# Kernel tuning notes

Hardware: AMD Instinct MI355X
Metric: run time of the kernel (lower is better)

The kernel has to match this reference:

```python
import jax, jax.numpy as jnp
import numpy as np
import math

H = 16
SEG = 128
DIL = 2


def hilbert_perm(M: int) -> jnp.ndarray:
    # Boustrophedon (snake) traversal of a ceil(sqrt(M)) grid, matching
    # create_hilbert_mapping_simple: skip linear positions >= M, keep first M.
    g = int(math.ceil(math.sqrt(M)))
    grid = np.arange(g * g).reshape(g, g)
    grid[1::2] = grid[1::2, ::-1]
    flat = grid.reshape(-1)
    flat = flat[flat < M][:M]
    return jnp.asarray(flat, dtype=jnp.int32)


def setup_inputs() -> dict:
    key = jax.random.key(0)
    kx, kq, ko = jax.random.split(key, 3)
    B, M, D = 4, 4096, 1024
    x = jax.random.normal(kx, (B, M, D), dtype=jnp.float32)
    # nn.Linear weights: [out_features, in_features], y = x @ W.T
    w_qkv = jax.random.normal(kq, (3 * D, D), dtype=jnp.float32) * (D ** -0.5)
    w_out = jax.random.normal(ko, (D, D), dtype=jnp.float32) * (D ** -0.5)
    return {"x": x, "w_qkv": w_qkv, "w_out": w_out}


def reference(x, w_qkv, w_out):
    B, M, Dm = x.shape
    hd = Dm // H
    scale = hd ** -0.5
    S = M // SEG  # number of segments (M chosen as a multiple of SEG)

    qkv = x @ w_qkv.T                              # [B, M, 3*Dm]
    qkv = qkv.reshape(B, M, 3, H, hd)
    q = qkv[:, :, 0].transpose(0, 2, 1, 3)         # [B, H, M, hd]
    k = qkv[:, :, 1].transpose(0, 2, 1, 3)
    v = qkv[:, :, 2].transpose(0, 2, 1, 3)

    perm = hilbert_perm(M)
    qh = q[:, :, perm]                             # Hilbert-reordered
    kh = k[:, :, perm]
    vh = v[:, :, perm]

    # segment-local dilated attention: each query attends to keys at
    # positions seg_start + j*DIL within its own segment
    qh = qh.reshape(B, H, S, SEG, hd)
    kd = kh.reshape(B, H, S, SEG, hd)[:, :, :, ::DIL]   # [B,H,S,SEG//DIL,hd]
    vd = vh.reshape(B, H, S, SEG, hd)[:, :, :, ::DIL]

    scores = jnp.einsum('bhsqd,bhskd->bhsqk', qh * scale, kd)
    attn = jax.nn.softmax(scores, axis=-1)
    o = jnp.einsum('bhsqk,bhskd->bhsqd', attn, vd)       # [B,H,S,SEG,hd]
    o = o.reshape(B, H, M, hd).transpose(0, 2, 1, 3).reshape(B, M, Dm)
    return o @ w_out.T
```

## Files before the change

kernel.cpp:

```cpp
#include <hip/hip_runtime.h>


typedef _Float16 f16x8 __attribute__((ext_vector_type(8)));
typedef _Float16 f16x4 __attribute__((ext_vector_type(4)));
typedef float f32x4 __attribute__((ext_vector_type(4)));

__device__ __forceinline__ int hperm(int i) {
  int r = i >> 6, c = i & 63;
  return (r << 6) | ((r & 1) ? (63 - c) : c);
}
__device__ __forceinline__ int arow_gather(int mp) {
  int b = mp >> 11, i = mp & 2047;
  int s = i >> 6, j = i & 63;
  return b * 4096 + hperm(s * 128 + 2 * j);
}
__device__ __forceinline__ void gload_lds16(const _Float16* g, _Float16* l) {
  __builtin_amdgcn_global_load_lds(
      (const __attribute__((address_space(1))) void*)g,
      (__attribute__((address_space(3))) void*)l, 16, 0, 0);
}

__global__ __launch_bounds__(256) void cast_all(
    const float* __restrict__ x, _Float16* __restrict__ xh,
    const float* __restrict__ wq, _Float16* __restrict__ wqh,
    const float* __restrict__ wo, _Float16* __restrict__ woh) {
  for (int i = blockIdx.x * 256 + threadIdx.x; i < 5242880; i += 256 * 2048) {
    const float* s;
    _Float16* d;
    int j;
    if (i < 4194304) {
      s = x; d = xh; j = i;
    } else if (i < 4980736) {
      s = wq; d = wqh; j = i - 4194304;
    } else {
      s = wo; d = woh; j = i - 4980736;
    }
    float4 v = ((const float4*)s)[j];
    f16x4 o;
    o[0] = (_Float16)v.x;
    o[1] = (_Float16)v.y;
    o[2] = (_Float16)v.z;
    o[3] = (_Float16)v.w;
    *(f16x4*)&d[(size_t)j * 4] = o;
  }
}


#define BAR __builtin_amdgcn_s_barrier()
#define LGKM_(n)                                            \
  do {                                                      \
    asm volatile("s_waitcnt lgkmcnt(" #n ")" ::: "memory"); \
    __builtin_amdgcn_sched_barrier(0);                      \
  } while (0)
#define VM4 asm volatile("s_waitcnt vmcnt(4)" ::: "memory")
#define VM0 asm volatile("s_waitcnt vmcnt(0)" ::: "memory")

#define STG(mat, kt, h, buf)                                               \
  do {                                                                     \
    const _Float16* g0 = ((mat) ? gpB : gpA)[(h)*2] + (size_t)(kt)*64;     \
    const _Float16* g1 = ((mat) ? gpB : gpA)[(h)*2 + 1] + (size_t)(kt)*64; \
    _Float16* d_ = &lds[buf][mat][h][t * 8];                               \
    gload_lds16(g0, d_);                                                   \
    gload_lds16(g1, d_ + 4096);                                            \
  } while (0)

#define LDA_K(buf, mh, ks)                                     \
  _Pragma("unroll") for (int m = 0; m < 4; m++) a[ks][m] =     \
      *(const f16x8*)(aB[buf][ks] + (mh)*4096 + m * 1024);

#define LDB_K(buf, nh, ks)                                           \
  _Pragma("unroll") for (int nf = 0; nf < 2; nf++) b[nh][ks][nf] =   \
      *(const f16x8*)(bB[buf][ks] + (nh)*2048 + nf * 1024);

#define MMH(mh, nh, ks)                                                     \
  _Pragma("unroll") for (int m = 0; m < 4; m++)                             \
      _Pragma("unroll") for (int nf = 0; nf < 2; nf++)                      \
          acc[(mh)*4 + m][(nh)*2 + nf] =                                    \
              __builtin_amdgcn_mfma_f32_16x16x32_f16(                       \
                  a[ks][m], b[nh][ks][nf], acc[(mh)*4 + m][(nh)*2 + nf],    \
                  0, 0, 0);

#define STQ(mh, nh)                                                        \
  _Pragma("unroll") for (int mf = 0; mf < 4; mf++) {                       \
    size_t row0 = arow0 + wm * 128 + ((mh)*4 + mf) * 16 + lg * 4;          \
    _Pragma("unroll") for (int nf = 0; nf < 2; nf++) {                     \
      size_t col = brow0 + wn * 64 + ((nh)*2 + nf) * 16 + lr;              \
      _Pragma("unroll") for (int j = 0; j < 4; j++) {                      \
        OutT v_ = (OutT)acc[(mh)*4 + mf][(nh)*2 + nf][j];                  \
        if constexpr (NT)                                                  \
          __builtin_nontemporal_store(v_, &C[(row0 + j) * N + col]);       \
        else                                                               \
          C[(row0 + j) * N + col] = v_;                                    \
      }                                                                    \
    }                                                                      \
  }

template <typename OutT, bool NT>
__device__ __forceinline__ void gemm_body(
    const _Float16* const* gpA, const _Float16* const* gpB,
    OutT* __restrict__ C, int N, size_t arow0, size_t brow0,
    _Float16 (&lds)[2][2][2][8192]) {
  const int t = threadIdx.x;
  const int lane = t & 63, wave = t >> 6;
  const int wm = wave >> 2, wn = wave & 3;
  const int lr = lane & 15, lg = lane >> 4;

  const int cx0 = (lg * 8) ^ ((lr & 7) << 3);
  const int cx1 = cx0 ^ 32;
  const _Float16* aB[2][2];
  const _Float16* bB[2][2];
#pragma unroll
  for (int bf = 0; bf < 2; bf++) {
    aB[bf][0] = &lds[bf][0][wm][lr * 64 + cx0];
    aB[bf][1] = &lds[bf][0][wm][lr * 64 + cx1];
    bB[bf][0] = &lds[bf][1][wn >> 1][(wn & 1) * 4096 + lr * 64 + cx0];
    bB[bf][1] = &lds[bf][1][wn >> 1][(wn & 1) * 4096 + lr * 64 + cx1];
  }

  f32x4 acc[8][4] = {};
  f16x8 a[2][4], b[2][2][2];

  STG(0, 0, 0, 0);
  STG(0, 0, 1, 0);
  STG(1, 0, 0, 0);
  STG(1, 0, 1, 0);
  STG(1, 1, 0, 1);
  STG(1, 1, 1, 1);
  VM4;
  BAR;

  for (int i = 0; i < 7; i++) {
    const int k1 = 2 * i + 1, k2 = 2 * i + 2, k3 = 2 * i + 3;
    LDA_K(0, 0, 0); LDB_K(0, 0, 0); LDA_K(0, 0, 1); LDB_K(0, 0, 1);
    STG(0, k1, 0, 1); BAR; LGKM_(6); MMH(0, 0, 0); LGKM_(0); MMH(0, 0, 1);
    LDB_K(0, 1, 0); LDB_K(0, 1, 1);
    STG(0, k1, 1, 1); BAR; LGKM_(2); MMH(0, 1, 0); LGKM_(0); MMH(0, 1, 1);
    LDA_K(0, 1, 0); LDA_K(0, 1, 1);
    STG(1, k2, 0, 0); BAR; LGKM_(4); MMH(1, 1, 0); LGKM_(0); MMH(1, 1, 1);
    STG(1, k2, 1, 0); VM4; BAR; MMH(1, 0, 0); MMH(1, 0, 1);
    LDA_K(1, 0, 0); LDB_K(1, 0, 0); LDA_K(1, 0, 1); LDB_K(1, 0, 1);
    STG(0, k2, 0, 0); BAR; LGKM_(6); MMH(0, 0, 0); LGKM_(0); MMH(0, 0, 1);
    LDB_K(1, 1, 0); LDB_K(1, 1, 1);
    STG(0, k2, 1, 0); BAR; LGKM_(2); MMH(0, 1, 0); LGKM_(0); MMH(0, 1, 1);
    LDA_K(1, 1, 0); LDA_K(1, 1, 1);
    STG(1, k3, 0, 1); BAR; LGKM_(4); MMH(1, 1, 0); LGKM_(0); MMH(1, 1, 1);
    STG(1, k3, 1, 1); VM4; BAR; MMH(1, 0, 0); MMH(1, 0, 1);
  }

  {
    LDA_K(0, 0, 0); LDB_K(0, 0, 0); LDA_K(0, 0, 1); LDB_K(0, 0, 1);
    STG(0, 15, 0, 1); BAR; LGKM_(6); MMH(0, 0, 0); LGKM_(0); MMH(0, 0, 1);
    LDB_K(0, 1, 0); LDB_K(0, 1, 1);
    STG(0, 15, 1, 1); BAR; LGKM_(2); MMH(0, 1, 0); LGKM_(0); MMH(0, 1, 1);
    LDA_K(0, 1, 0); LDA_K(0, 1, 1);
    BAR; LGKM_(4); MMH(1, 1, 0); LGKM_(0); MMH(1, 1, 1);
    VM0; BAR; MMH(1, 0, 0); MMH(1, 0, 1);
    LDA_K(1, 0, 0); LDB_K(1, 0, 0); LDA_K(1, 0, 1); LDB_K(1, 0, 1);
    BAR; LGKM_(6); MMH(0, 0, 0); LGKM_(0); MMH(0, 0, 1);
    STQ(0, 0);
    LDB_K(1, 1, 0); LDB_K(1, 1, 1);
    BAR; LGKM_(2); MMH(0, 1, 0); LGKM_(0); MMH(0, 1, 1);
    STQ(0, 1);
    LDA_K(1, 1, 0); LDA_K(1, 1, 1);
    BAR; LGKM_(4); MMH(1, 1, 0); LGKM_(0); MMH(1, 1, 1);
    STQ(1, 1);
    MMH(1, 0, 0); MMH(1, 0, 1);
    STQ(1, 0);
  }
}

__global__ __launch_bounds__(512, 2) void gemm_qkv8(
    const _Float16* __restrict__ xh, const _Float16* __restrict__ wqh,
    _Float16* __restrict__ qh, _Float16* __restrict__ kvh) {
  __shared__ _Float16 lds[2][2][2][8192];
  const int t = threadIdx.x;
  const int id = blockIdx.x;
  const int sw = (id & 7) * (gridDim.x >> 3) + (id >> 3);
  const bool iskv = sw >= 256;
  const int wid = iskv ? sw - 256 : sw;
  const int N = iskv ? 2048 : 1024;
  const int bn = iskv ? (wid & 7) : (wid & 3);
  const int bm = iskv ? (wid >> 3) : (wid >> 2);
  const _Float16* Bw = wqh + (iskv ? (size_t)1048576 : 0);
  _Float16* C = iskv ? kvh : qh;

  const int sgrow = t >> 3;
  const int sgcol = ((t & 7) * 8) ^ ((sgrow & 7) << 3);
  const _Float16* gpA[4];
  const _Float16* gpB[4];
#pragma unroll
  for (int r = 0; r < 4; r++) {
    int mr = bm * 256 + 64 * r + sgrow;
    int ar = iskv ? arow_gather(mr) : mr;
    gpA[r] = xh + (size_t)ar * 1024 + sgcol;
    gpB[r] = Bw + ((size_t)bn * 256 + 64 * r + sgrow) * 1024 + sgcol;
  }
  gemm_body<_Float16, false>(gpA, gpB, C, N, (size_t)bm * 256,
                             (size_t)bn * 256, lds);
}

__global__ __launch_bounds__(512, 2) void gemm_out8(
    const _Float16* __restrict__ atth, const _Float16* __restrict__ woh,
    float* __restrict__ out) {
  __shared__ _Float16 lds[2][2][2][8192];
  const int t = threadIdx.x;
  const int id = blockIdx.x;
  const int sw = (id & 7) * (gridDim.x >> 3) + (id >> 3);
  const int bn = sw & 3, bm = sw >> 2;

  const int sgrow = t >> 3;
  const int sgcol = ((t & 7) * 8) ^ ((sgrow & 7) << 3);
  const _Float16* gpA[4];
  const _Float16* gpB[4];
#pragma unroll
  for (int r = 0; r < 4; r++) {
    gpA[r] = atth + ((size_t)bm * 256 + 64 * r + sgrow) * 1024 + sgcol;
    gpB[r] = woh + ((size_t)bn * 256 + 64 * r + sgrow) * 1024 + sgcol;
  }
  gemm_body<float, true>(gpA, gpB, out, 1024, (size_t)bm * 256,
                         (size_t)bn * 256, lds);
}

#define STRD 72

__global__ __launch_bounds__(256) void hilbert_attn(
    const _Float16* __restrict__ qh, const _Float16* __restrict__ kvh,
    _Float16* __restrict__ aout) {
  __shared__ _Float16 Qs[128 * STRD];
  __shared__ _Float16 Ks[64 * STRD];
  __shared__ _Float16 Vt[64 * STRD];
  __shared__ _Float16 Ps[128 * STRD];
  const int blk = blockIdx.x;
  const int s = blk & 31, h = (blk >> 5) & 15, b = blk >> 9;
  const int t = threadIdx.x, lane = t & 63, wave = t >> 6;
  const int lr = lane & 15, lg = lane >> 4, lk = lg * 8;
  const int col = (t & 7) * 8, rr = t >> 3;
  const size_t kvb = ((size_t)b * 2048 + s * 64) * 2048;

#pragma unroll
  for (int i = 0; i < 4; i++) {
    int m = i * 32 + rr;
    int p = b * 4096 + hperm(s * 128 + m);
    *(f16x8*)&Qs[m * STRD + col] =
        *(const f16x8*)&qh[(size_t)p * 1024 + h * 64 + col];
  }
#pragma unroll
  for (int i = 0; i < 2; i++) {
    int j = i * 32 + rr;
    *(f16x8*)&Ks[j * STRD + col] =
        *(const f16x8*)&kvh[kvb + (size_t)j * 2048 + h * 64 + col];
    f16x8 vv =
        *(const f16x8*)&kvh[kvb + (size_t)j * 2048 + 1024 + h * 64 + col];
#pragma unroll
    for (int e = 0; e < 8; e++) Vt[(col + e) * STRD + j] = vv[e];
  }
  __syncthreads();

  f32x4 accs[2][4] = {};
#pragma unroll
  for (int kk = 0; kk < 2; kk++) {
    f16x8 aa[2], bb[4];
#pragma unroll
    for (int m = 0; m < 2; m++)
      aa[m] = *(const f16x8*)&Qs[(wave * 32 + m * 16 + lr) * STRD + kk * 32 + lk];
#pragma unroll
    for (int n = 0; n < 4; n++)
      bb[n] = *(const f16x8*)&Ks[(n * 16 + lr) * STRD + kk * 32 + lk];
#pragma unroll
    for (int m = 0; m < 2; m++)
#pragma unroll
      for (int n = 0; n < 4; n++)
        accs[m][n] =
            __builtin_amdgcn_mfma_f32_16x16x32_f16(aa[m], bb[n], accs[m][n], 0, 0, 0);
  }

#pragma unroll
  for (int m = 0; m < 2; m++) {
#pragma unroll
    for (int j = 0; j < 4; j++) {
      float sc0 = accs[m][0][j] * 0.125f;
      float sc1 = accs[m][1][j] * 0.125f;
      float sc2 = accs[m][2][j] * 0.125f;
      float sc3 = accs[m][3][j] * 0.125f;
      float mx = fmaxf(fmaxf(sc0, sc1), fmaxf(sc2, sc3));
#pragma unroll
      for (int d = 1; d < 16; d <<= 1) mx = fmaxf(mx, __shfl_xor(mx, d, 16));
      float e0 = __expf(sc0 - mx), e1 = __expf(sc1 - mx);
      float e2 = __expf(sc2 - mx), e3 = __expf(sc3 - mx);
      float sum = (e0 + e1) + (e2 + e3);
#pragma unroll
      for (int d = 1; d < 16; d <<= 1) sum += __shfl_xor(sum, d, 16);
      float inv = 1.0f / sum;
      int row = wave * 32 + m * 16 + lg * 4 + j;
      Ps[row * STRD + 0 * 16 + lr] = (_Float16)(e0 * inv);
      Ps[row * STRD + 1 * 16 + lr] = (_Float16)(e1 * inv);
      Ps[row * STRD + 2 * 16 + lr] = (_Float16)(e2 * inv);
      Ps[row * STRD + 3 * 16 + lr] = (_Float16)(e3 * inv);
    }
  }
  __syncthreads();

  f32x4 acco[2][4] = {};
#pragma unroll
  for (int kk = 0; kk < 2; kk++) {
    f16x8 aa[2], bb[4];
#pragma unroll
    for (int m = 0; m < 2; m++)
      aa[m] = *(const f16x8*)&Ps[(wave * 32 + m * 16 + lr) * STRD + kk * 32 + lk];
#pragma unroll
    for (int n = 0; n < 4; n++)
      bb[n] = *(const f16x8*)&Vt[(n * 16 + lr) * STRD + kk * 32 + lk];
#pragma unroll
    for (int m = 0; m < 2; m++)
#pragma unroll
      for (int n = 0; n < 4; n++)
        acco[m][n] =
            __builtin_amdgcn_mfma_f32_16x16x32_f16(aa[m], bb[n], acco[m][n], 0, 0, 0);
  }

  const size_t orow0 = (size_t)b * 4096 + s * 128;
#pragma unroll
  for (int m = 0; m < 2; m++) {
#pragma unroll
    for (int n = 0; n < 4; n++) {
#pragma unroll
      for (int j = 0; j < 4; j++) {
        size_t row = orow0 + wave * 32 + m * 16 + lg * 4 + j;
        aout[row * 1024 + h * 64 + n * 16 + lr] = (_Float16)acco[m][n][j];
      }
    }
  }
}

extern "C" void kernel_launch(void* const* d_in, const int* in_sizes, int n_in,
                              void* d_out, int out_size, void* d_ws, size_t ws_size,
                              hipStream_t stream) {
  const float* x = (const float*)d_in[0];
  const float* w_qkv = (const float*)d_in[1];
  const float* w_out = (const float*)d_in[2];
  float* out = (float*)d_out;
  char* ws = (char*)d_ws;

  _Float16* xh = (_Float16*)(ws + 0);
  _Float16* wqh = (_Float16*)(ws + (size_t)33554432);
  _Float16* woh = (_Float16*)(ws + (size_t)39845888);
  _Float16* qh = (_Float16*)(ws + (size_t)41943040);
  _Float16* kvh = (_Float16*)(ws + (size_t)75497472);
  _Float16* atth = (_Float16*)(ws + (size_t)109051904);

  cast_all<<<2048, 256, 0, stream>>>(x, xh, w_qkv, wqh, w_out, woh);

  gemm_qkv8<<<512, 512, 0, stream>>>(xh, wqh, qh, kvh);
  hilbert_attn<<<2048, 256, 0, stream>>>(qh, kvh, atth);
  gemm_out8<<<256, 512, 0, stream>>>(atth, woh, out);
}
```

Baseline: 154.2 us.

## Restructure GEMM main loop into two phases with fewer barriers

Regroups the GEMM k-loop from eight sub-phases per iteration into four larger phases. Each phase issues all LDS fragment reads up front, pinned in order with sched barriers, and waits on them with staggered lgkmcnt counts. The global-to-LDS staging for both halves now runs back to back before a single barrier, halving the number of s_barriers per k-step. The aim is to cut barrier sync overhead and overlap LDS reads with MFMAs more deeply, at the cost of more live fragment registers and a changed ordering of LDS buffer reuse that could create hazards.

Measured after the change: 155.4 us. No clear change (+0.8%).

```diff
diff --git a/kernel.cpp b/kernel.cpp
--- a/kernel.cpp
+++ b/kernel.cpp
@@ -47,10 +47,11 @@
 
 
 #define BAR __builtin_amdgcn_s_barrier()
+#define SB0 __builtin_amdgcn_sched_barrier(0)
 #define LGKM_(n)                                            \
   do {                                                      \
     asm volatile("s_waitcnt lgkmcnt(" #n ")" ::: "memory"); \
-    __builtin_amdgcn_sched_barrier(0);                      \
+    SB0;                                                    \
   } while (0)
 #define VM4 asm volatile("s_waitcnt vmcnt(4)" ::: "memory")
 #define VM0 asm volatile("s_waitcnt vmcnt(0)" ::: "memory")
@@ -79,6 +80,32 @@
               __builtin_amdgcn_mfma_f32_16x16x32_f16(                       \
                   a[ks][m], b[nh][ks][nf], acc[(mh)*4 + m][(nh)*2 + nf],    \
                   0, 0, 0);
+
+#define PH_A(rb, kt, sb, DOSTG)                              \
+  do {                                                       \
+    LDA_K(rb, 0, 0); LDB_K(rb, 0, 0); SB0;                   \
+    LDA_K(rb, 0, 1); LDB_K(rb, 0, 1); SB0;                   \
+    LDB_K(rb, 1, 0); SB0;                                    \
+    LDB_K(rb, 1, 1); SB0;                                    \
+    if (DOSTG) { STG(0, kt, 0, sb); STG(0, kt, 1, sb); }     \
+    BAR;                                                     \
+    LGKM_(10); MMH(0, 0, 0);                                 \
+    LGKM_(4);  MMH(0, 0, 1);                                 \
+    LGKM_(2);  MMH(0, 1, 0);                                 \
+    LGKM_(0);  MMH(0, 1, 1);                                 \
+  } while (0)
+
+#define PH_B(rb, kt, sb, DOSTG, VMW)                         \
+  do {                                                       \
+    LDA_K(rb, 1, 0); SB0;                                    \
+    LDA_K(rb, 1, 1); SB0;                                    \
+    if (DOSTG) { STG(1, kt, 0, sb); STG(1, kt, 1, sb); }     \
+    VMW;                                                     \
+    BAR;                                                     \
+    LGKM_(4); MMH(1, 1, 0);                                  \
+    LGKM_(0); MMH(1, 1, 1);                                  \
+    MMH(1, 0, 0); MMH(1, 0, 1);                              \
+  } while (0)
 
 #define STQ(mh, nh)                                                        \
   _Pragma("unroll") for (int mf = 0; mf < 4; mf++) {                       \
@@ -131,38 +158,33 @@
 
   for (int i = 0; i < 7; i++) {
     const int k1 = 2 * i + 1, k2 = 2 * i + 2, k3 = 2 * i + 3;
-    LDA_K(0, 0, 0); LDB_K(0, 0, 0); LDA_K(0, 0, 1); LDB_K(0, 0, 1);
-    STG(0, k1, 0, 1); BAR; LGKM_(6); MMH(0, 0, 0); LGKM_(0); MMH(0, 0, 1);
-    LDB_K(0, 1, 0); LDB_K(0, 1, 1);
-    STG(0, k1, 1, 1); BAR; LGKM_(2); MMH(0, 1, 0); LGKM_(0); MMH(0, 1, 1);
-    LDA_K(0, 1, 0); LDA_K(0, 1, 1);
-    STG(1, k2, 0, 0); BAR; LGKM_(4); MMH(1, 1, 0); LGKM_(0); MMH(1, 1, 1);
-    STG(1, k2, 1, 0); VM4; BAR; MMH(1, 0, 0); MMH(1, 0, 1);
-    LDA_K(1, 0, 0); LDB_K(1, 0, 0); LDA_K(1, 0, 1); LDB_K(1, 0, 1);
-    STG(0, k2, 0, 0); BAR; LGKM_(6); MMH(0, 0, 0); LGKM_(0); MMH(0, 0, 1);
-    LDB_K(1, 1, 0); LDB_K(1, 1, 1);
-    STG(0, k2, 1, 0); BAR; LGKM_(2); MMH(0, 1, 0); LGKM_(0); MMH(0, 1, 1);
-    LDA_K(1, 1, 0); LDA_K(1, 1, 1);
-    STG(1, k3, 0, 1); BAR; LGKM_(4); MMH(1, 1, 0); LGKM_(0); MMH(1, 1, 1);
-    STG(1, k3, 1, 1); VM4; BAR; MMH(1, 0, 0); MMH(1, 0, 1);
-  }
-
+    PH_A(0, k1, 1, 1);
+    PH_B(0, k2, 0, 1, VM4);
+    PH_A(1, k2, 0, 1);
+    PH_B(1, k3, 1, 1, VM4);
+  }
+
+  PH_A(0, 15, 1, 1);
+  PH_B(0, 0, 0, 0, VM0);
   {
-    LDA_K(0, 0, 0); LDB_K(0, 0, 0); LDA_K(0, 0, 1); LDB_K(0, 0, 1);
-    STG(0, 15, 0, 1); BAR; LGKM_(6); MMH(0, 0, 0); LGKM_(0); MMH(0, 0, 1);
-    LDB_K(0, 1, 0); LDB_K(0, 1, 1);
-    STG(0, 15, 1, 1); BAR; LGKM_(2); MMH(0, 1, 0); LGKM_(0); MMH(0, 1, 1);
-    LDA_K(0, 1, 0); LDA_K(0, 1, 1);
-    BAR; LGKM_(4); MMH(1, 1, 0); LGKM_(0); MMH(1, 1, 1);
-    VM0; BAR; MMH(1, 0, 0); MMH(1, 0, 1);
-    LDA_K(1, 0, 0); LDB_K(1, 0, 0); LDA_K(1, 0, 1); LDB_K(1, 0, 1);
-    BAR; LGKM_(6); MMH(0, 0, 0); LGKM_(0); MMH(0, 0, 1);
+    LDA_K(1, 0, 0); LDB_K(1, 0, 0); SB0;
+    LDA_K(1, 0, 1); LDB_K(1, 0, 1); SB0;
+    LDB_K(1, 1, 0); SB0;
+    LDB_K(1, 1, 1); SB0;
+    BAR;
+    LGKM_(10); MMH(0, 0, 0);
+    LGKM_(4);  MMH(0, 0, 1);
     STQ(0, 0);
-    LDB_K(1, 1, 0); LDB_K(1, 1, 1);
-    BAR; LGKM_(2); MMH(0, 1, 0); LGKM_(0); MMH(0, 1, 1);
+    LGKM_(2);  MMH(0, 1, 0);
+    LGKM_(0);  MMH(0, 1, 1);
     STQ(0, 1);
-    LDA_K(1, 1, 0); LDA_K(1, 1, 1);
-    BAR; LGKM_(4); MMH(1, 1, 0); LGKM_(0); MMH(1, 1, 1);
+  }
+  {
+    LDA_K(1, 1, 0); SB0;
+    LDA_K(1, 1, 1); SB0;
+    BAR;
+    LGKM_(4); MMH(1, 1, 0);
+    LGKM_(0); MMH(1, 1, 1);
     STQ(1, 1);
     MMH(1, 0, 0); MMH(1, 0, 1);
     STQ(1, 0);
```
